# Optimization experiments

Measured on AMD Instinct MI355X. Metric: run time of the kernel, lower is better.

Reference implementation:

```python
import jax, jax.numpy as jnp
import numpy as np

DIM = 1024
HEADS = 16
BLK = 129
DK = 64
DV = 64
B = 4
N = BLK * 32  # 4128


def setup_inputs() -> dict:
    key = jax.random.key(0)
    ks = jax.random.split(key, 6)
    inner_k = HEADS * DK
    inner_v = HEADS * DV
    s = 1.0 / np.sqrt(DIM)
    x = jax.random.normal(ks[0], (B, N, DIM), dtype=jnp.float32)
    Wq = jax.random.normal(ks[1], (inner_k, DIM), dtype=jnp.float32) * s
    Wk = jax.random.normal(ks[2], (inner_k, DIM), dtype=jnp.float32) * s
    Wv = jax.random.normal(ks[3], (inner_v, DIM), dtype=jnp.float32) * s
    Wo = jax.random.normal(ks[4], (DIM, inner_v), dtype=jnp.float32) * (1.0 / np.sqrt(inner_v))
    bo = jax.random.normal(ks[5], (DIM,), dtype=jnp.float32) * 0.01
    return {"x": x, "Wq": Wq, "Wk": Wk, "Wv": Wv, "Wo": Wo, "bo": bo}


def reference(x, Wq, Wk, Wv, Wo, bo):
    Bsz, Nlen, D = x.shape
    nb = Nlen // BLK
    scale = 1.0 / np.sqrt(DK)
    # projections (Linear without bias: x @ W.T)
    q = (x @ Wq.T).reshape(Bsz, nb, BLK, HEADS, DK)
    k = (x @ Wk.T).reshape(Bsz, nb, BLK, HEADS, DK)
    v = (x @ Wv.T).reshape(Bsz, nb, BLK, HEADS, DV)
    # block-local attention: each block attends within itself
    scores = jnp.einsum('bnqhd,bnkhd->bnhqk', q, k) * scale  # [B,nb,H,BLK,BLK]
    attn = jax.nn.softmax(scores, axis=-1)
    out_blk = jnp.einsum('bnhqk,bnkhd->bnhqd', attn, v)  # [B,nb,H,BLK,DV]
    # global attention among the first token of each block
    qg = q[:, :, 0]  # [B,nb,H,DK]
    kg = k[:, :, 0]
    vg = v[:, :, 0]
    sg = jnp.einsum('bqhd,bkhd->bhqk', qg, kg) * scale  # [B,H,nb,nb]
    ag = jax.nn.softmax(sg, axis=-1)
    out_g = jnp.einsum('bhqk,bkhd->bqhd', ag, vg)  # [B,nb,H,DV]
    # add global output onto position 0 of each block
    out_blk = out_blk.at[:, :, :, 0, :].add(out_g.transpose(0, 1, 2, 3).swapaxes(2, 2))  # out_g already [B,nb,H,DV]
    # reassemble to [B,N,H*DV]
    out = out_blk.transpose(0, 1, 3, 2, 4).reshape(Bsz, Nlen, HEADS * DV)
    return out @ Wo.T + bo
```

## Files before the change

### kernel.cpp

```cpp
#include <hip/hip_runtime.h>

typedef unsigned short u16;
typedef __attribute__((ext_vector_type(8))) __bf16 bf16x8;
typedef __attribute__((ext_vector_type(4))) float f32x4;
typedef __attribute__((ext_vector_type(8))) u16 u16x8;
typedef __attribute__((ext_vector_type(4))) u16 u16x4;

#define DIMSZ 1024
#define HEADS 16
#define BLKSZ 129
#define NBLK 32
#define NTOK (BLKSZ * NBLK)
#define BATCH 4
#define MROWS (BATCH * NTOK)

#define MFMA __builtin_amdgcn_mfma_f32_16x16x32_bf16

#define SSTR 152
#define KSTR 72

#define NKT 32

__device__ __forceinline__ float bf2f(u16 u) {
  return __uint_as_float(((unsigned)u) << 16);
}
__device__ __forceinline__ u16 f2bf(float f) {
  unsigned u = __float_as_uint(f);
  u += 0x7FFFu + ((u >> 16) & 1u);
  return (u16)(u >> 16);
}

#define GLD16(ldsp, gp) __builtin_amdgcn_global_load_lds( \
    (const __attribute__((address_space(1))) void*)(gp),   \
    (__attribute__((address_space(3))) void*)(ldsp), 16, 0, 0)

__global__ __launch_bounds__(256) void cast_f32_bf16(
    const float* __restrict__ in, u16* __restrict__ out, int n)
{
  int i = (blockIdx.x * 256 + threadIdx.x) * 4;
  if (i < n) {
    float4 f = *(const float4*)(in + i);
    u16x4 o = { f2bf(f.x), f2bf(f.y), f2bf(f.z), f2bf(f.w) };
    *(u16x4*)(out + i) = o;
  }
}

__global__ __launch_bounds__(256) void cast_w3(
    const float* __restrict__ a, const float* __restrict__ b,
    const float* __restrict__ c, u16* __restrict__ out)
{
  const int nw = DIMSZ * DIMSZ;
  int i = (blockIdx.x * 256 + threadIdx.x) * 4;
  const float* src = (i < nw) ? a : (i < 2 * nw ? b : c);
  int j = (i < nw) ? i : (i < 2 * nw ? i - nw : i - 2 * nw);
  float4 f = *(const float4*)(src + j);
  u16x4 o = { f2bf(f.x), f2bf(f.y), f2bf(f.z), f2bf(f.w) };
  *(u16x4*)(out + i) = o;
}

__device__ __forceinline__ int xcd_swz(int bid, int nwg) {
  const int xcd = bid & 7, l = bid >> 3;
  const int q = nwg >> 3, r = nwg & 7;
  return (xcd < r ? xcd * (q + 1) : r * (q + 1) + (xcd - r) * q) + l;
}

__device__ __forceinline__ void stage_sq(u16* slot, const u16* gA,
                                         const u16* gB, int tid) {
  GLD16(slot + tid * 8, gA);
  GLD16(slot + 2048 + tid * 8, gA + 64 * DIMSZ);
  GLD16(slot + 4096 + tid * 8, gB);
  GLD16(slot + 6144 + tid * 8, gB + 64 * DIMSZ);
}

__device__ __forceinline__ void gemm_pipe_sq(
    const u16* __restrict__ A, const u16* __restrict__ Bm,
    int m0, int n0, int tid, u16 (*sm)[8192], f32x4 (*acc)[4])
{
  const int lane = tid & 63, w = tid >> 6;
  const int qd = lane >> 4, l15 = lane & 15;
  const int wm = (w >> 1) * 64, wn = (w & 1) * 64;
  const int qdsw = (qd ^ ((l15 >> 1) & 3)) * 8;

  const int srow = tid >> 2;
  const int schk = (tid & 3) ^ ((tid >> 3) & 3);
  const u16* gA = A + (size_t)(m0 + srow) * DIMSZ + schk * 8;
  const u16* gB = Bm + (size_t)(n0 + srow) * DIMSZ + schk * 8;

  u16 *p0 = sm[0], *p1 = sm[1], *p2 = sm[2];

  stage_sq(p0, gA, gB, tid);
  stage_sq(p1, gA + 32, gB + 32, tid);
  asm volatile("s_waitcnt vmcnt(4)" ::: "memory");
  __builtin_amdgcn_s_barrier();
  __builtin_amdgcn_sched_barrier(0);

  for (int t = 0; t < NKT; ++t) {
    if (t + 2 < NKT)
      stage_sq(p2, gA + (t + 2) * 32, gB + (t + 2) * 32, tid);

    bf16x8 af[4], bv[4];
#pragma unroll
    for (int mi = 0; mi < 4; ++mi)
      af[mi] = *(const bf16x8*)&p0[(wm + mi * 16 + l15) * 32 + qdsw];
#pragma unroll
    for (int ni = 0; ni < 4; ++ni)
      bv[ni] = *(const bf16x8*)&p0[4096 + (wn + ni * 16 + l15) * 32 + qdsw];

    __builtin_amdgcn_s_setprio(1);
#pragma unroll
    for (int mi = 0; mi < 4; ++mi)
#pragma unroll
      for (int ni = 0; ni < 4; ++ni)
        acc[mi][ni] = MFMA(af[mi], bv[ni], acc[mi][ni], 0, 0, 0);
    __builtin_amdgcn_s_setprio(0);

    __builtin_amdgcn_sched_barrier(0);
    if (t + 2 < NKT) {
      asm volatile("s_waitcnt vmcnt(4)" ::: "memory");
    } else {
      asm volatile("s_waitcnt vmcnt(0)" ::: "memory");
    }
    __builtin_amdgcn_s_barrier();
    __builtin_amdgcn_sched_barrier(0);

    u16* tmp = p0; p0 = p1; p1 = p2; p2 = tmp;
  }
}

__global__ __launch_bounds__(256, 3) void gemm_qkv(
    const u16* __restrict__ A, const u16* __restrict__ B,
    u16* __restrict__ Cq, u16* __restrict__ Ck, u16* __restrict__ Cv)
{
  __shared__ u16 sm[3][8192];
  const int tid = threadIdx.x;
  f32x4 acc[4][4];
#pragma unroll
  for (int mi = 0; mi < 4; ++mi)
#pragma unroll
    for (int ni = 0; ni < 4; ++ni)
      acc[mi][ni] = (f32x4){0.f, 0.f, 0.f, 0.f};

  const int wg = xcd_swz(blockIdx.x, 129 * 24);
  const int nt = wg % 24, mt = wg / 24;
  const int m0 = mt * 128, n0 = nt * 128;

  gemm_pipe_sq(A, B, m0, n0, tid, sm, acc);

  u16* C = nt < 8 ? Cq : (nt < 16 ? Ck : Cv);
  const int c0 = (nt & 7) * 128;
  const int lane = tid & 63, w = tid >> 6;
  const int qd = lane >> 4, l15 = lane & 15;
  const int wm = (w >> 1) * 64, wn = (w & 1) * 64;
#pragma unroll
  for (int mi = 0; mi < 4; ++mi)
#pragma unroll
    for (int ni = 0; ni < 4; ++ni) {
      const int row0 = m0 + wm + mi * 16 + qd * 4;
      const int col  = c0 + wn + ni * 16 + l15;
#pragma unroll
      for (int r = 0; r < 4; ++r)
        C[(size_t)(row0 + r) * DIMSZ + col] = f2bf(acc[mi][ni][r]);
    }
}

__global__ __launch_bounds__(256, 3) void gemm_out(
    const u16* __restrict__ A, const u16* __restrict__ B,
    float* __restrict__ C, const float* __restrict__ bias)
{
  __shared__ u16 sm[3][8192];
  const int tid = threadIdx.x;
  f32x4 acc[4][4];
#pragma unroll
  for (int mi = 0; mi < 4; ++mi)
#pragma unroll
    for (int ni = 0; ni < 4; ++ni)
      acc[mi][ni] = (f32x4){0.f, 0.f, 0.f, 0.f};

  const int wg = xcd_swz(blockIdx.x, 129 * 8);
  const int nt = wg & 7, mt = wg >> 3;
  const int m0 = mt * 128, n0 = nt * 128;

  gemm_pipe_sq(A, B, m0, n0, tid, sm, acc);

  const int lane = tid & 63, w = tid >> 6;
  const int qd = lane >> 4, l15 = lane & 15;
  const int wm = (w >> 1) * 64, wn = (w & 1) * 64;
#pragma unroll
  for (int mi = 0; mi < 4; ++mi)
#pragma unroll
    for (int ni = 0; ni < 4; ++ni) {
      const int row0 = m0 + wm + mi * 16 + qd * 4;
      const int col  = n0 + wn + ni * 16 + l15;
      float badd = bias[col];
#pragma unroll
      for (int r = 0; r < 4; ++r)
        C[(size_t)(row0 + r) * DIMSZ + col] = acc[mi][ni][r] + badd;
    }
}

__global__ __launch_bounds__(256) void global_attn(
    const u16* __restrict__ q, const u16* __restrict__ k,
    const u16* __restrict__ v, float* __restrict__ g)
{
  __shared__ float sQ[NBLK * 64];
  __shared__ float sKT[64 * NBLK];
  __shared__ float sV[NBLK * 64];
  __shared__ float sp[4][NBLK];
  const int b = blockIdx.x >> 4, h = blockIdx.x & 15;
  const int tid = threadIdx.x, lane = tid & 63, w = tid >> 6;

  for (int idx = tid; idx < NBLK * 64; idx += 256) {
    int j = idx >> 6, d = idx & 63;
    size_t off = ((size_t)(b * NTOK + j * BLKSZ)) * DIMSZ + h * 64 + d;
    sQ[idx] = bf2f(q[off]);
    sKT[d * NBLK + j] = bf2f(k[off]);
    sV[idx] = bf2f(v[off]);
  }
  __syncthreads();

  for (int i = w; i < NBLK; i += 4) {
    float s = -3.0e38f;
    if (lane < 32) {
      float acc = 0.f;
      for (int d = 0; d < 64; ++d) acc += sQ[i * 64 + d] * sKT[d * NBLK + lane];
      s = acc * 0.125f;
    }
    float m = s;
    for (int t = 1; t < 64; t <<= 1) m = fmaxf(m, __shfl_xor(m, t));
    float e = (lane < 32) ? __expf(s - m) : 0.f;
    float sum = e;
    for (int t = 1; t < 64; t <<= 1) sum += __shfl_xor(sum, t);
    if (lane < 32) sp[w][lane] = e / sum;
    asm volatile("s_waitcnt lgkmcnt(0)" ::: "memory");
    float acc = 0.f;
    for (int jj = 0; jj < NBLK; ++jj) acc += sp[w][jj] * sV[jj * 64 + lane];
    g[(((size_t)b * NBLK + i) * HEADS + h) * 64 + lane] = acc;
  }
}

__global__ __launch_bounds__(512) void block_attn(
    const u16* q, const u16* __restrict__ k,
    const u16* __restrict__ v, const float* __restrict__ g,
    u16* ao)
{
  __shared__ u16 sS[144 * SSTR];
  __shared__ u16 sKV[144 * KSTR];
  const int b = blockIdx.x, blk = blockIdx.y, h = blockIdx.z;
  const int tid = threadIdx.x, lane = tid & 63, w = tid >> 6;
  const int qd = lane >> 4, l15 = lane & 15;
  const int h64 = h * 64;
  const size_t row_base = (size_t)b * NTOK + (size_t)blk * BLKSZ;
  const f32x4 zero4 = {0.f, 0.f, 0.f, 0.f};

  {
    const u16x8 zero8 = {0, 0, 0, 0, 0, 0, 0, 0};
    for (int c = tid; c < 144 * 8; c += 512) {
      int row = c >> 3, cc = c & 7;
      u16x8 val = zero8;
      if (row < BLKSZ)
        val = *(const u16x8*)(k + (row_base + row) * DIMSZ + h64 + cc * 8);
      *(u16x8*)&sKV[row * KSTR + cc * 8] = val;
    }
  }
  __syncthreads();

  {
    const int tbeg = w * 10;
    const int tend = (w == 7) ? 81 : tbeg + 10;
    int cur_mt = -1;
    bf16x8 qf0, qf1;
    for (int t = tbeg; t < tend; ++t) {
      int mt = t / 9, nt = t - mt * 9;
      if (mt != cur_mt) {
        cur_mt = mt;
        int qrow = mt * 16 + l15;
        if (qrow > 128) qrow = 128;
        const u16* qp = q + (row_base + qrow) * DIMSZ + h64;
        qf0 = *(const bf16x8*)(qp + qd * 8);
        qf1 = *(const bf16x8*)(qp + 32 + qd * 8);
      }
      bf16x8 kf0 = *(const bf16x8*)&sKV[(nt * 16 + l15) * KSTR + qd * 8];
      bf16x8 kf1 = *(const bf16x8*)&sKV[(nt * 16 + l15) * KSTR + 32 + qd * 8];
      f32x4 c = zero4;
      c = MFMA(qf0, kf0, c, 0, 0, 0);
      c = MFMA(qf1, kf1, c, 0, 0, 0);
      int r0 = mt * 16 + qd * 4, col = nt * 16 + l15;
#pragma unroll
      for (int r = 0; r < 4; ++r)
        sS[(r0 + r) * SSTR + col] = f2bf(c[r] * 0.125f);
    }
  }
  __syncthreads();

  for (int c = tid; c < BLKSZ * 8; c += 512) {
    int row = c >> 3, cc = c & 7;
    u16x8 val = *(const u16x8*)(v + (row_base + row) * DIMSZ + h64 + cc * 8);
#pragma unroll
    for (int jj = 0; jj < 8; ++jj)
      sKV[(cc * 8 + jj) * SSTR + row] = val[jj];
  }

  for (int row = w; row < BLKSZ; row += 8) {
    float x1 = bf2f(sS[row * SSTR + lane]);
    float x2 = bf2f(sS[row * SSTR + 64 + lane]);
    float x3 = (lane == 0) ? bf2f(sS[row * SSTR + 128]) : -3.0e38f;
    float m = fmaxf(fmaxf(x1, x2), x3);
    for (int t = 1; t < 64; t <<= 1) m = fmaxf(m, __shfl_xor(m, t));
    float e1 = __expf(x1 - m), e2 = __expf(x2 - m);
    float e3 = (lane == 0) ? __expf(x3 - m) : 0.f;
    float s = e1 + e2 + e3;
    for (int t = 1; t < 64; t <<= 1) s += __shfl_xor(s, t);
    float inv = 1.f / s;
    sS[row * SSTR + lane] = f2bf(e1 * inv);
    sS[row * SSTR + 64 + lane] = f2bf(e2 * inv);
    if (lane == 0) sS[row * SSTR + 128] = f2bf(e3 * inv);
  }
  __syncthreads();

  for (int t = w; t < 36; t += 8) {
    int mt = t >> 2, nt = t & 3;
    f32x4 c = zero4;
#pragma unroll
    for (int kk = 0; kk < 128; kk += 32) {
      bf16x8 pf = *(const bf16x8*)&sS[(mt * 16 + l15) * SSTR + kk + qd * 8];
      bf16x8 vf = *(const bf16x8*)&sKV[(nt * 16 + l15) * SSTR + kk + qd * 8];
      c = MFMA(pf, vf, c, 0, 0, 0);
    }
    int dv = nt * 16 + l15;
    float v128 = bf2f(sKV[dv * SSTR + 128]);
    int r0 = mt * 16 + qd * 4;
#pragma unroll
    for (int r = 0; r < 4; ++r) {
      int row = r0 + r;
      if (row < BLKSZ) {
        float p128 = bf2f(sS[row * SSTR + 128]);
        float val = c[r] + p128 * v128;
        if (row == 0)
          val += g[(((size_t)b * NBLK + blk) * HEADS + h) * 64 + dv];
        ao[(row_base + row) * DIMSZ + h64 + dv] = f2bf(val);
      }
    }
  }
}

extern "C" void kernel_launch(void* const* d_in, const int* in_sizes, int n_in,
                              void* d_out, int out_size, void* d_ws, size_t ws_size,
                              hipStream_t stream) {
  const float* x  = (const float*)d_in[0];
  const float* Wq = (const float*)d_in[1];
  const float* Wk = (const float*)d_in[2];
  const float* Wv = (const float*)d_in[3];
  const float* Wo = (const float*)d_in[4];
  const float* bo = (const float*)d_in[5];
  float* out = (float*)d_out;

  char* ws = (char*)d_ws;
  const size_t xb = (size_t)MROWS * DIMSZ * sizeof(u16);
  float* gb     = (float*)ws;
  u16*   qb     = (u16*)(ws + (1u << 20));
  u16*   x16    = (u16*)(ws + (1u << 20) + xb);
  u16*   Wqkv16 = (u16*)(ws + (1u << 20) + 2 * xb);
  u16*   Wo16   = x16;
  u16*   kb     = (u16*)d_out;
  u16*   vb     = (u16*)d_out + (size_t)MROWS * DIMSZ;

  const int nx = MROWS * DIMSZ;
  const int nw = DIMSZ * DIMSZ;
  cast_f32_bf16<<<nx / 1024, 256, 0, stream>>>(x, x16, nx);
  cast_w3<<<3 * nw / 1024, 256, 0, stream>>>(Wq, Wk, Wv, Wqkv16);

  gemm_qkv<<<dim3(129 * 24), 256, 0, stream>>>(x16, Wqkv16, qb, kb, vb);

  cast_f32_bf16<<<nw / 1024, 256, 0, stream>>>(Wo, Wo16, nw);

  global_attn<<<dim3(BATCH * HEADS), 256, 0, stream>>>(qb, kb, vb, gb);
  block_attn<<<dim3(BATCH, NBLK, HEADS), 512, 0, stream>>>(qb, kb, vb, gb, qb);
  gemm_out<<<dim3(129 * 8), 256, 0, stream>>>(qb, Wo16, out, bo);
}
```

Before: 400.1 us.

## Enlarge QKV GEMM tiles to 256x256 with 512-thread workgroups

Replaces the 128x128-tile, 256-thread QKV projection GEMM with a 256x256-tile, 512-thread version. Each wave computes a 128x64 sub-tile, and staging uses a 4-slot LDS ring (128 KB) with a K-step of 32 and two stages in flight. The goal is to cut global and L2 traffic per FLOP through more operand reuse. In exchange, one workgroup per CU is likely the LDS limit, the grid is much smaller (780 blocks) with a tail wave, and the last row tile reads past the end of the activation matrix, so stores need guarding.

```diff
diff --git a/kernel.cpp b/kernel.cpp
--- a/kernel.cpp
+++ b/kernel.cpp
@@ -20,6 +20,7 @@
 #define KSTR 72
 
 #define NKT 32
+#define NPH 32
 
 __device__ __forceinline__ float bf2f(u16 u) {
   return __uint_as_float(((unsigned)u) << 16);
@@ -64,6 +65,109 @@
   return (xcd < r ? xcd * (q + 1) : r * (q + 1) + (xcd - r) * q) + l;
 }
 
+__device__ __forceinline__ void stage_pair(u16* slot, const u16* gA1,
+                                           const u16* gB1, int k0, int tid) {
+  GLD16(slot + tid * 8, gA1 + k0);
+  GLD16(slot + 4096 + tid * 8, gA1 + 128 * DIMSZ + k0);
+  GLD16(slot + 8192 + tid * 8, gB1 + k0);
+  GLD16(slot + 12288 + tid * 8, gB1 + 128 * DIMSZ + k0);
+}
+
+__device__ __forceinline__ void gemm_pipe256(
+    const u16* __restrict__ A, const u16* __restrict__ Bm,
+    int m0, int n0, int tid, u16 (*sm)[16384], f32x4 (*acc)[4])
+{
+  const int lane = tid & 63, w = tid >> 6;
+  const int qd = lane >> 4, l15 = lane & 15;
+  const int wm = (w >> 2) * 128, wn = (w & 3) * 64;
+  const int qdsw = (qd ^ ((l15 >> 1) & 3)) * 8;
+
+  const int srow = tid >> 2;
+  const int schk = (tid & 3) ^ ((tid >> 3) & 3);
+  const u16* gA1 = A + (size_t)(m0 + srow) * DIMSZ + schk * 8;
+  const u16* gB1 = Bm + (size_t)(n0 + srow) * DIMSZ + schk * 8;
+
+  stage_pair(sm[0], gA1, gB1, 0, tid);
+  stage_pair(sm[1], gA1, gB1, 32, tid);
+  asm volatile("s_waitcnt vmcnt(4)" ::: "memory");
+  __builtin_amdgcn_s_barrier();
+  __builtin_amdgcn_sched_barrier(0);
+
+#pragma unroll 4
+  for (int g = 0; g < NPH; ++g) {
+    const u16* sA = sm[g & 3];
+    const u16* sB = sm[g & 3] + 8192;
+
+    bf16x8 af[8], bv[4];
+#pragma unroll
+    for (int mi = 0; mi < 8; ++mi)
+      af[mi] = *(const bf16x8*)&sA[(wm + mi * 16 + l15) * 32 + qdsw];
+#pragma unroll
+    for (int ni = 0; ni < 4; ++ni)
+      bv[ni] = *(const bf16x8*)&sB[(wn + ni * 16 + l15) * 32 + qdsw];
+
+    if (g + 2 < NPH)
+      stage_pair(sm[(g + 2) & 3], gA1, gB1, (g + 2) * 32, tid);
+
+    __builtin_amdgcn_sched_barrier(0);
+    __builtin_amdgcn_s_barrier();
+
+    __builtin_amdgcn_s_setprio(1);
+#pragma unroll
+    for (int mi = 0; mi < 8; ++mi)
+#pragma unroll
+      for (int ni = 0; ni < 4; ++ni)
+        acc[mi][ni] = MFMA(af[mi], bv[ni], acc[mi][ni], 0, 0, 0);
+    __builtin_amdgcn_s_setprio(0);
+    __builtin_amdgcn_sched_barrier(0);
+
+    if (g + 2 < NPH) {
+      asm volatile("s_waitcnt vmcnt(4)" ::: "memory");
+    } else if (g + 1 < NPH) {
+      asm volatile("s_waitcnt vmcnt(0)" ::: "memory");
+    }
+    __builtin_amdgcn_s_barrier();
+    __builtin_amdgcn_sched_barrier(0);
+  }
+}
+
+__global__ __launch_bounds__(512, 2) void gemm_qkv(
+    const u16* __restrict__ A, const u16* __restrict__ B,
+    u16* __restrict__ Cq, u16* __restrict__ Ck, u16* __restrict__ Cv)
+{
+  __shared__ u16 sm[4][16384];
+  const int tid = threadIdx.x;
+  f32x4 acc[8][4];
+#pragma unroll
+  for (int mi = 0; mi < 8; ++mi)
+#pragma unroll
+    for (int ni = 0; ni < 4; ++ni)
+      acc[mi][ni] = (f32x4){0.f, 0.f, 0.f, 0.f};
+
+  const int wg = xcd_swz(blockIdx.x, 65 * 12);
+  const int nt = wg % 12, mt = wg / 12;
+  const int m0 = mt * 256, n0 = nt * 256;
+
+  gemm_pipe256(A, B, m0, n0, tid, sm, acc);
+
+  u16* C = nt < 4 ? Cq : (nt < 8 ? Ck : Cv);
+  const int c0 = (nt & 3) * 256;
+  const int lane = tid & 63, w = tid >> 6;
+  const int qd = lane >> 4, l15 = lane & 15;
+  const int wm = (w >> 2) * 128, wn = (w & 3) * 64;
+#pragma unroll
+  for (int mi = 0; mi < 8; ++mi)
+#pragma unroll
+    for (int ni = 0; ni < 4; ++ni) {
+      const int row0 = m0 + wm + mi * 16 + qd * 4;
+      const int col  = c0 + wn + ni * 16 + l15;
+#pragma unroll
+      for (int r = 0; r < 4; ++r)
+        if (row0 + r < MROWS)
+          C[(size_t)(row0 + r) * DIMSZ + col] = f2bf(acc[mi][ni][r]);
+    }
+}
+
 __device__ __forceinline__ void stage_sq(u16* slot, const u16* gA,
                                          const u16* gB, int tid) {
   GLD16(slot + tid * 8, gA);
@@ -125,42 +229,6 @@
 
     u16* tmp = p0; p0 = p1; p1 = p2; p2 = tmp;
   }
-}
-
-__global__ __launch_bounds__(256, 3) void gemm_qkv(
-    const u16* __restrict__ A, const u16* __restrict__ B,
-    u16* __restrict__ Cq, u16* __restrict__ Ck, u16* __restrict__ Cv)
-{
-  __shared__ u16 sm[3][8192];
-  const int tid = threadIdx.x;
-  f32x4 acc[4][4];
-#pragma unroll
-  for (int mi = 0; mi < 4; ++mi)
-#pragma unroll
-    for (int ni = 0; ni < 4; ++ni)
-      acc[mi][ni] = (f32x4){0.f, 0.f, 0.f, 0.f};
-
-  const int wg = xcd_swz(blockIdx.x, 129 * 24);
-  const int nt = wg % 24, mt = wg / 24;
-  const int m0 = mt * 128, n0 = nt * 128;
-
-  gemm_pipe_sq(A, B, m0, n0, tid, sm, acc);
-
-  u16* C = nt < 8 ? Cq : (nt < 16 ? Ck : Cv);
-  const int c0 = (nt & 7) * 128;
-  const int lane = tid & 63, w = tid >> 6;
-  const int qd = lane >> 4, l15 = lane & 15;
-  const int wm = (w >> 1) * 64, wn = (w & 1) * 64;
-#pragma unroll
-  for (int mi = 0; mi < 4; ++mi)
-#pragma unroll
-    for (int ni = 0; ni < 4; ++ni) {
-      const int row0 = m0 + wm + mi * 16 + qd * 4;
-      const int col  = c0 + wn + ni * 16 + l15;
-#pragma unroll
-      for (int r = 0; r < 4; ++r)
-        C[(size_t)(row0 + r) * DIMSZ + col] = f2bf(acc[mi][ni][r]);
-    }
 }
 
 __global__ __launch_bounds__(256, 3) void gemm_out(
@@ -369,7 +437,7 @@
   cast_f32_bf16<<<nx / 1024, 256, 0, stream>>>(x, x16, nx);
   cast_w3<<<3 * nw / 1024, 256, 0, stream>>>(Wq, Wk, Wv, Wqkv16);
 
-  gemm_qkv<<<dim3(129 * 24), 256, 0, stream>>>(x16, Wqkv16, qb, kb, vb);
+  gemm_qkv<<<dim3(65 * 12), 512, 0, stream>>>(x16, Wqkv16, qb, kb, vb);
 
   cast_f32_bf16<<<nw / 1024, 256, 0, stream>>>(Wo, Wo16, nw);
 
```

After: 404.6 us. No clear change (+1.1%).
